# Kernel tuning notes

Hardware: AMD Instinct MI355X
Metric: run time of the kernel (lower is better)

The kernel has to match this reference:

```python
import jax, jax.numpy as jnp
import numpy as np

N = 16384          # nodes
E = 262144         # edges (before self-loops)
FIN_N, FIN_E = 768, 64
F, FE = 256, 128   # node/edge channels
H, C = 8, 32       # heads, per-head dim (H*C == F)
L = 2              # num GATv2 modules
NEG_SLOPE = 0.2


def layer_norm(x, g, b, eps=1e-5):
    mu = jnp.mean(x, axis=-1, keepdims=True)
    var = jnp.mean((x - mu) ** 2, axis=-1, keepdims=True)
    return (x - mu) * jax.lax.rsqrt(var + eps) * g + b


def segment_softmax(logits, seg, n):
    # logits: [Et, H], seg: [Et] destination node ids
    m = jax.ops.segment_max(logits, seg, num_segments=n)
    m = jnp.where(jnp.isfinite(m), m, 0.0)
    e = jnp.exp(logits - m[seg])
    s = jax.ops.segment_sum(e, seg, num_segments=n)
    return e / (s[seg] + 1e-16)


def setup_inputs() -> dict:
    key = jax.random.key(0)
    ks = jax.random.split(key, 20)
    inp = {
        "node_feats": jax.random.normal(ks[0], (N, FIN_N), jnp.float32),
        "edge_index": jax.random.randint(ks[1], (2, E), 0, N, dtype=jnp.int32),
        "edge_attr": jax.random.normal(ks[2], (E, FIN_E), jnp.float32),
        # input projections (bias=False)
        "init_node_w": jax.random.normal(ks[3], (F, FIN_N), jnp.float32) * 0.02,
        "init_edge_w": jax.random.normal(ks[4], (FE, FIN_E), jnp.float32) * 0.02,
        # per-layer GATv2 params, stacked on leading layer dim L
        "lin_l_w": jax.random.normal(ks[5], (L, H * C, F), jnp.float32) * 0.05,
        "lin_l_b": jnp.zeros((L, H * C), jnp.float32),
        "lin_r_w": jax.random.normal(ks[6], (L, H * C, F), jnp.float32) * 0.05,
        "lin_r_b": jnp.zeros((L, H * C), jnp.float32),
        "lin_edge_w": jax.random.normal(ks[7], (L, H * C, FE), jnp.float32) * 0.05,
        "att": jax.random.normal(ks[8], (L, H, C), jnp.float32) * 0.05,
        "gat_bias": jnp.zeros((L, H * C), jnp.float32),
        # block params
        "ln1_g": jnp.ones((L, F), jnp.float32), "ln1_b": jnp.zeros((L, F), jnp.float32),
        "mlp_w1": jax.random.normal(ks[9], (L, 2 * F, F), jnp.float32) * 0.05,
        "mlp_w2": jax.random.normal(ks[10], (L, F, 2 * F), jnp.float32) * 0.05,
        "ln2_g": jnp.ones((L, F), jnp.float32), "ln2_b": jnp.zeros((L, F), jnp.float32),
    }
    return inp


def _gatv2_module(x, src, dst, e_emb, p, l, n):
    # e_emb: [Et, H, C] already projected edge embeddings (incl. self-loops)
    x_l = (x @ p["lin_l_w"][l].T + p["lin_l_b"][l]).reshape(n, H, C)
    x_r = (x @ p["lin_r_w"][l].T + p["lin_r_b"][l]).reshape(n, H, C)
    m = x_l[src] + x_r[dst] + e_emb                    # [Et, H, C]
    g = jnp.where(m >= 0, m, NEG_SLOPE * m)            # leaky_relu(0.2)
    logits = jnp.einsum('ehc,hc->eh', g, p["att"][l])
    alpha = segment_softmax(logits, dst, n)            # [Et, H]
    out = jax.ops.segment_sum(alpha[:, :, None] * x_l[src], dst, num_segments=n)
    out = out.reshape(n, H * C) + p["gat_bias"][l]
    # residual -> LN -> MLP -> residual -> LN  (dropout=0, eval mode)
    h = layer_norm(x + out, p["ln1_g"][l], p["ln1_b"][l])
    y = jax.nn.gelu(h @ p["mlp_w1"][l].T, approximate=False) @ p["mlp_w2"][l].T
    return layer_norm(h + y, p["ln2_g"][l], p["ln2_b"][l])


def reference(node_feats, edge_index, edge_attr, init_node_w, init_edge_w,
              lin_l_w, lin_l_b, lin_r_w, lin_r_b, lin_edge_w, att, gat_bias,
              ln1_g, ln1_b, mlp_w1, mlp_w2, ln2_g, ln2_b):
    p = dict(lin_l_w=lin_l_w, lin_l_b=lin_l_b, lin_r_w=lin_r_w, lin_r_b=lin_r_b,
             lin_edge_w=lin_edge_w, att=att, gat_bias=gat_bias, ln1_g=ln1_g,
             ln1_b=ln1_b, mlp_w1=mlp_w1, mlp_w2=mlp_w2, ln2_g=ln2_g, ln2_b=ln2_b)
    x = node_feats @ init_node_w.T                     # [N, F]
    ea = edge_attr @ init_edge_w.T                     # [E, FE]
    src, dst = edge_index[0], edge_index[1]
    # add self loops with fill_value='mean' (mean of incoming edge_attr per node)
    cnt = jax.ops.segment_sum(jnp.ones((E,), ea.dtype), dst, num_segments=N)
    loop_attr = jax.ops.segment_sum(ea, dst, num_segments=N) / jnp.maximum(cnt, 1.0)[:, None]
    ea_all = jnp.concatenate([ea, loop_attr], axis=0)  # [E+N, FE]
    ar = jnp.arange(N, dtype=src.dtype)
    src_all = jnp.concatenate([src, ar])
    dst_all = jnp.concatenate([dst, ar])
    for l in range(L):
        e_emb = (ea_all @ lin_edge_w[l].T).reshape(-1, H, C)
        x = _gatv2_module(x, src_all, dst_all, e_emb, p, l, N)
    return x
```

## Files before the change

### kernel.cpp

```cpp
#include <hip/hip_runtime.h>

typedef unsigned short u16;
typedef __attribute__((ext_vector_type(8))) short s8v;
typedef __attribute__((ext_vector_type(4))) float f4v;

#define NN 16384
#define EE 262144
#define ET (EE + NN)
#define NTILES (ET / 64)

__device__ __forceinline__ float bfu(u16 h){ return __uint_as_float((unsigned)h << 16); }
__device__ __forceinline__ u16 f2bf(float f){
  unsigned u = __float_as_uint(f);
  unsigned r = u + 0x7FFFu + ((u >> 16) & 1u);
  return (u16)(r >> 16);
}
__device__ __forceinline__ float ldf(const void* p, size_t i, int isbf){
  return isbf ? bfu(((const u16*)p)[i]) : ((const float*)p)[i];
}
__device__ __forceinline__ float gelu_f(float x){ return 0.5f*x*(1.0f+erff(x*0.7071067811865475f)); }

__device__ __forceinline__ uint4 load8bf(const void* p, size_t eoff, int isbf){
  if (isbf) return *(const uint4*)((const u16*)p + eoff);
  const float* f = (const float*)p + eoff;
  uint4 r;
  r.x = (unsigned)f2bf(f[0]) | ((unsigned)f2bf(f[1])<<16);
  r.y = (unsigned)f2bf(f[2]) | ((unsigned)f2bf(f[3])<<16);
  r.z = (unsigned)f2bf(f[4]) | ((unsigned)f2bf(f[5])<<16);
  r.w = (unsigned)f2bf(f[6]) | ((unsigned)f2bf(f[7])<<16);
  return r;
}

__global__ void k_detect(const void* nf, int* flag)
{
  int t = threadIdx.x;
  const float* f = (const float*)nf;
  int cnt = 0;
  for (int i = t; i < 4096; i += 256) {
    float a = fabsf(f[i]);
    if (a > 1e-5f && a < 100.0f) cnt++;
  }
  __shared__ int s[256];
  s[t] = cnt; __syncthreads();
  for (int st = 128; st > 0; st >>= 1) { if (t < st) s[t] += s[t+st]; __syncthreads(); }
  if (t == 0) *flag = (s[0] < 2048) ? 1 : 0;
}

template<int ACT, int CFMT>
__global__ __launch_bounds__(256)
void mfma_gemm(const void* __restrict__ A, int a_fmt,
               const void* __restrict__ B1, size_t b1off,
               const void* __restrict__ B2, size_t b2off, int nsplit,
               const void* __restrict__ bias1, const void* __restrict__ bias2,
               size_t bioff, int has_bias,
               void* __restrict__ C, int M, int N, int K,
               const int* __restrict__ dflag)
{
  int isbf = *dflag;
  int af = (a_fmt == 2) ? isbf : a_fmt;
  __shared__ u16 As[128*40];
  __shared__ u16 Bs[128*40];
  int bm = blockIdx.y*128, bn = blockIdx.x*128;
  int t = threadIdx.x;
  int w = t>>6, lane = t&63, l4 = lane&15, quad = lane>>4;
  int wm = w>>1, wn = w&1;
  f4v zero = {0.f,0.f,0.f,0.f};
  f4v acc[4][4];
  #pragma unroll
  for (int i=0;i<4;i++)
    #pragma unroll
    for (int j=0;j<4;j++) acc[i][j] = zero;

  for (int k0 = 0; k0 < K; k0 += 32) {
    __syncthreads();
    #pragma unroll
    for (int it = 0; it < 2; ++it) {
      int sid = t + it*256;
      int row = sid >> 2, sk = sid & 3;
      *(uint4*)&As[row*40 + sk*8] = load8bf(A, (size_t)(bm+row)*K + k0 + sk*8, af);
      int col = bn + row;
      uint4 vb;
      if (col < nsplit) vb = load8bf(B1, b1off + (size_t)col*K + k0 + sk*8, isbf);
      else              vb = load8bf(B2, b2off + (size_t)(col-nsplit)*K + k0 + sk*8, isbf);
      *(uint4*)&Bs[row*40 + sk*8] = vb;
    }
    __syncthreads();
    s8v a[4], b[4];
    #pragma unroll
    for (int i=0;i<4;i++) a[i] = *(const s8v*)&As[(wm*64 + i*16 + l4)*40 + quad*8];
    #pragma unroll
    for (int j=0;j<4;j++) b[j] = *(const s8v*)&Bs[(wn*64 + j*16 + l4)*40 + quad*8];
    #pragma unroll
    for (int i=0;i<4;i++)
      #pragma unroll
      for (int j=0;j<4;j++)
        acc[i][j] = __builtin_amdgcn_mfma_f32_16x16x32_bf16(a[i], b[j], acc[i][j], 0,0,0);
  }
  #pragma unroll
  for (int i=0;i<4;i++)
    #pragma unroll
    for (int j=0;j<4;j++) {
      int col = bn + wn*64 + j*16 + l4;
      float bv = 0.f;
      if (has_bias) bv = (col < nsplit) ? ldf(bias1, bioff + col, isbf)
                                        : ldf(bias2, bioff + col - nsplit, isbf);
      #pragma unroll
      for (int r=0;r<4;r++) {
        int row = bm + wm*64 + i*16 + quad*4 + r;
        float v = acc[i][j][r] + bv;
        if (ACT==1) v = gelu_f(v);
        if (CFMT==1) ((u16*)C)[(size_t)row*N + col] = f2bf(v);
        else         ((float*)C)[(size_t)row*N + col] = v;
      }
    }
}

__global__ void k_count(const int* __restrict__ dst, int* __restrict__ deg)
{
  int e = blockIdx.x*256 + threadIdx.x;
  if (e >= ET) return;
  int d = (e < EE) ? dst[e] : (e - EE);
  atomicAdd(&deg[d], 1);
}

__global__ void k_scan(const int* __restrict__ deg, int* __restrict__ rowstart)
{
  __shared__ int csum[256];
  int t = threadIdx.x;
  int s = 0;
  for (int i=0;i<64;i++) s += deg[t*64+i];
  csum[t] = s;
  __syncthreads();
  if (t == 0) {
    int r = 0;
    for (int i=0;i<256;i++){ int v = csum[i]; csum[i] = r; r += v; }
    rowstart[NN] = r;
  }
  __syncthreads();
  int b = csum[t];
  for (int i=0;i<64;i++){ rowstart[t*64+i] = b; b += deg[t*64+i]; }
}

__global__ void k_scatter(const int* __restrict__ dst, const int* __restrict__ rowstart,
                          int* __restrict__ fill, int* __restrict__ csr)
{
  int e = blockIdx.x*256 + threadIdx.x;
  if (e >= ET) return;
  int d = (e < EE) ? dst[e] : (e - EE);
  int pos = rowstart[d] + atomicAdd(&fill[d], 1);
  csr[pos] = e;
}

__global__ void k_loopmean(const int* __restrict__ csr, const int* __restrict__ rowstart,
                           const void* __restrict__ edge_attr, u16* __restrict__ loopmean,
                           const int* __restrict__ dflag)
{
  int isbf = *dflag;
  int n = blockIdx.x, j = threadIdx.x;
  int s = rowstart[n], e1 = rowstart[n+1];
  float sum = 0.f; int cnt = 0;
  for (int p = s; p < e1; ++p) {
    int eid = csr[p];
    if (eid < EE) { sum += ldf(edge_attr, (size_t)eid*64 + j, isbf); cnt++; }
  }
  loopmean[(size_t)n*64 + j] = f2bf(sum / (float)max(cnt, 1));
}

__global__ void k_wc(const void* __restrict__ We, const void* __restrict__ iew,
                     u16* __restrict__ Wcb, const int* __restrict__ dflag)
{
  int isbf = *dflag;
  int idx = blockIdx.x*256 + threadIdx.x;
  int j = idx & 63, c = (idx >> 6) & 255, l = idx >> 14;
  float s = 0.f;
  for (int k=0;k<128;k++) s += ldf(We, ((size_t)l*256 + c)*128 + k, isbf) * ldf(iew, (size_t)k*64 + j, isbf);
  Wcb[idx] = f2bf(s);
}

__global__ __launch_bounds__(256)
void k_elogits(const int* __restrict__ src, const int* __restrict__ dst,
               const u16* __restrict__ Wcb, const u16* __restrict__ xlr,
               const void* __restrict__ edge_attr, const u16* __restrict__ loopmean,
               const void* __restrict__ att, size_t att_off,
               float* __restrict__ logits, const int* __restrict__ dflag)
{
  int isbf = *dflag;
  __shared__ u16 WcF[32*64*8];
  __shared__ u16 attr_s[64*72];
  __shared__ float satt[256];
  __shared__ int ssrc[64], sdst[64];

  int t = threadIdx.x;
  int w = t>>6, lane = t&63, l4 = lane&15, quad = lane>>4;

  satt[t] = ldf(att, att_off + t, isbf);
  #pragma unroll
  for (int f = 0; f < 8; ++f) {
    int fr = w + f*4;
    int i = fr >> 1, ks = fr & 1;
    *(uint4*)&WcF[(fr*64 + lane)*8] = *(const uint4*)&Wcb[(size_t)(16*i + l4)*64 + ks*32 + quad*8];
  }

  f4v zero = {0.f,0.f,0.f,0.f};
  for (int tile = blockIdx.x; tile < NTILES; tile += gridDim.x) {
    int e0 = tile*64;
    __syncthreads();
    if (t < 64) {
      int e = e0 + t;
      ssrc[t] = (e < EE) ? src[e] : (e - EE);
      sdst[t] = (e < EE) ? dst[e] : (e - EE);
    }
    {
      int er = t >> 2, part = t & 3;
      int e = e0 + er;
      uint4 v0, v1;
      if (e < EE) {
        v0 = load8bf(edge_attr, (size_t)e*64 + part*16,     isbf);
        v1 = load8bf(edge_attr, (size_t)e*64 + part*16 + 8, isbf);
      } else {
        v0 = *(const uint4*)&loopmean[(size_t)(e-EE)*64 + part*16];
        v1 = *(const uint4*)&loopmean[(size_t)(e-EE)*64 + part*16 + 8];
      }
      *(uint4*)&attr_s[er*72 + part*16]     = v0;
      *(uint4*)&attr_s[er*72 + part*16 + 8] = v1;
    }
    __syncthreads();

    s8v b0 = *(const s8v*)&attr_s[(w*16 + l4)*72 + quad*8];
    s8v b1 = *(const s8v*)&attr_s[(w*16 + l4)*72 + 32 + quad*8];
    f4v acc[16];
    #pragma unroll
    for (int i=0;i<16;++i){
      s8v a0 = *(const s8v*)&WcF[((2*i  )*64 + lane)*8];
      s8v a1 = *(const s8v*)&WcF[((2*i+1)*64 + lane)*8];
      acc[i] = __builtin_amdgcn_mfma_f32_16x16x32_bf16(a0, b0, zero, 0,0,0);
      acc[i] = __builtin_amdgcn_mfma_f32_16x16x32_bf16(a1, b1, acc[i], 0,0,0);
    }

    int me = w*16 + l4;
    int sn = ssrc[me], dn = sdst[me];
    float ph[8] = {0.f,0.f,0.f,0.f,0.f,0.f,0.f,0.f};
    #pragma unroll
    for (int i=0;i<16;++i){
      uint2 xlv = *(const uint2*)&xlr[(size_t)sn*512 +       i*16 + quad*4];
      uint2 xrv = *(const uint2*)&xlr[(size_t)dn*512 + 256 + i*16 + quad*4];
      float4 av = *(const float4*)&satt[i*16 + quad*4];
      float m0 = acc[i][0] + bfu((u16)(xlv.x & 0xffff)) + bfu((u16)(xrv.x & 0xffff));
      float m1 = acc[i][1] + bfu((u16)(xlv.x >> 16))    + bfu((u16)(xrv.x >> 16));
      float m2 = acc[i][2] + bfu((u16)(xlv.y & 0xffff)) + bfu((u16)(xrv.y & 0xffff));
      float m3 = acc[i][3] + bfu((u16)(xlv.y >> 16))    + bfu((u16)(xrv.y >> 16));
      float g0 = fmaxf(m0, 0.2f*m0), g1 = fmaxf(m1, 0.2f*m1);
      float g2 = fmaxf(m2, 0.2f*m2), g3 = fmaxf(m3, 0.2f*m3);
      ph[i>>1] += av.x*g0 + av.y*g1 + av.z*g2 + av.w*g3;
    }
    #pragma unroll
    for (int h=0;h<8;++h){
      ph[h] += __shfl_xor(ph[h], 16);
      ph[h] += __shfl_xor(ph[h], 32);
    }
    if (quad == 0){
      float4 lo = {ph[0], ph[1], ph[2], ph[3]};
      float4 hi = {ph[4], ph[5], ph[6], ph[7]};
      *(float4*)&logits[(size_t)(e0 + me)*8]     = lo;
      *(float4*)&logits[(size_t)(e0 + me)*8 + 4] = hi;
    }
  }
}

__global__ __launch_bounds__(256)
void k_aggln(const int* __restrict__ csr, const int* __restrict__ rowstart, const int* __restrict__ src,
             const float* __restrict__ logits, const u16* __restrict__ xlr, const float* __restrict__ xbuf,
             const void* __restrict__ gat_bias, const void* __restrict__ ln1g, const void* __restrict__ ln1b,
             size_t poff, float* __restrict__ hbuf, const int* __restrict__ dflag)
{
  int isbf = *dflag;
  int lane = threadIdx.x & 63, wid = threadIdx.x >> 6;
  int n = blockIdx.x*4 + wid;
  int s = rowstart[n], deg = rowstart[n+1] - s;
  int myh = lane >> 3;
  float mrun = -3.0e38f, lrun = 0.f;
  float a0=0.f, a1=0.f, a2=0.f, a3=0.f;

  for (int c0 = 0; c0 < deg; c0 += 64) {
    int idx = s + c0 + lane; if (idx >= ET) idx = ET-1;
    int ev = csr[idx];
    int sv = (ev < EE) ? src[ev] : (ev - EE);
    int lim = min(64, deg - c0);
    for (int j = 0; j < lim; ++j) {
      int eid = __shfl(ev, j);
      int sn  = __shfl(sv, j);
      float lg = logits[(size_t)eid*8 + myh];
      uint2 xv = *(const uint2*)&xlr[(size_t)sn*512 + 4*lane];
      float mn = fmaxf(mrun, lg);
      float sc = __expf(mrun - mn);
      float wv = __expf(lg - mn);
      mrun = mn;
      lrun = lrun*sc + wv;
      a0 = a0*sc + wv*bfu((u16)(xv.x & 0xffff));
      a1 = a1*sc + wv*bfu((u16)(xv.x >> 16));
      a2 = a2*sc + wv*bfu((u16)(xv.y & 0xffff));
      a3 = a3*sc + wv*bfu((u16)(xv.y >> 16));
    }
  }
  float inv = 1.f/(lrun + 1e-16f);
  int c = 4*lane;
  float4 res = *(const float4*)&xbuf[(size_t)n*256 + c];
  float o0 = a0*inv + ldf(gat_bias, poff+c+0, isbf) + res.x;
  float o1 = a1*inv + ldf(gat_bias, poff+c+1, isbf) + res.y;
  float o2 = a2*inv + ldf(gat_bias, poff+c+2, isbf) + res.z;
  float o3 = a3*inv + ldf(gat_bias, poff+c+3, isbf) + res.w;

  float v = o0+o1+o2+o3;
  #pragma unroll
  for (int off=1; off<64; off<<=1) v += __shfl_xor(v, off);
  float mu = v * (1.f/256.f);
  float d0=o0-mu, d1=o1-mu, d2=o2-mu, d3=o3-mu;
  float v2 = d0*d0+d1*d1+d2*d2+d3*d3;
  #pragma unroll
  for (int off=1; off<64; off<<=1) v2 += __shfl_xor(v2, off);
  float wn = rsqrtf(v2*(1.f/256.f) + 1e-5f);
  float4 outv;
  outv.x = d0*wn*ldf(ln1g, poff+c+0, isbf) + ldf(ln1b, poff+c+0, isbf);
  outv.y = d1*wn*ldf(ln1g, poff+c+1, isbf) + ldf(ln1b, poff+c+1, isbf);
  outv.z = d2*wn*ldf(ln1g, poff+c+2, isbf) + ldf(ln1b, poff+c+2, isbf);
  outv.w = d3*wn*ldf(ln1g, poff+c+3, isbf) + ldf(ln1b, poff+c+3, isbf);
  *(float4*)&hbuf[(size_t)n*256 + c] = outv;
}

__global__ __launch_bounds__(256)
void k_ln_add(const float* __restrict__ a, const u16* __restrict__ b2,
              const void* __restrict__ gg, const void* __restrict__ bb, size_t poff,
              float* __restrict__ out, const int* __restrict__ dflag)
{
  int isbf = *dflag;
  int n = blockIdx.x, t = threadIdx.x;
  __shared__ float r[256];
  float x = a[(size_t)n*256 + t] + bfu(b2[(size_t)n*256 + t]);
  r[t] = x; __syncthreads();
  for (int st = 128; st > 0; st >>= 1) { if (t < st) r[t] += r[t+st]; __syncthreads(); }
  float mu = r[0] * (1.f/256.f);
  __syncthreads();
  float d = x - mu;
  r[t] = d*d; __syncthreads();
  for (int st = 128; st > 0; st >>= 1) { if (t < st) r[t] += r[t+st]; __syncthreads(); }
  float var = r[0] * (1.f/256.f);
  out[(size_t)n*256 + t] = d * rsqrtf(var + 1e-5f) * ldf(gg, poff + t, isbf) + ldf(bb, poff + t, isbf);
}

__global__ void k_out(const float* __restrict__ x, void* __restrict__ out, const int* __restrict__ dflag)
{
  int isbf = *dflag;
  int i = blockIdx.x*256 + threadIdx.x;
  if (isbf) ((u16*)out)[i] = f2bf(x[i]);
  else      ((float*)out)[i] = x[i];
}

extern "C" void kernel_launch(void* const* d_in, const int* in_sizes, int n_in,
                              void* d_out, int out_size, void* d_ws, size_t ws_size,
                              hipStream_t stream)
{
  const void* node_feats = d_in[0];
  const int*  edge_index = (const int*)d_in[1];
  const void* edge_attr  = d_in[2];
  const void* init_node_w= d_in[3];
  const void* init_edge_w= d_in[4];
  const void* lin_l_w    = d_in[5];
  const void* lin_l_b    = d_in[6];
  const void* lin_r_w    = d_in[7];
  const void* lin_r_b    = d_in[8];
  const void* lin_edge_w = d_in[9];
  const void* att        = d_in[10];
  const void* gat_bias   = d_in[11];
  const void* ln1_g      = d_in[12];
  const void* ln1_b      = d_in[13];
  const void* mlp_w1     = d_in[14];
  const void* mlp_w2     = d_in[15];
  const void* ln2_g      = d_in[16];
  const void* ln2_b      = d_in[17];

  const int* srcp = edge_index;
  const int* dstp = edge_index + EE;

  char* p = (char*)d_ws;
  auto alloc = [&](size_t bytes) { void* r = (void*)p; p += (bytes + 255) & ~(size_t)255; return r; };
  int*   dflag   = (int*)alloc(256);
  int*   deg     = (int*)alloc((size_t)NN*4);
  int*   rowstart= (int*)alloc((size_t)(NN+1)*4);
  int*   fill    = (int*)alloc((size_t)NN*4);
  int*   csr     = (int*)alloc((size_t)ET*4);
  u16*   Wcb     = (u16*)alloc((size_t)2*256*64*2);
  u16*   loopmean= (u16*)alloc((size_t)NN*64*2);
  float* logits  = (float*)alloc((size_t)ET*8*4);
  float* xbuf    = (float*)alloc((size_t)NN*256*4);
  float* hbuf    = (float*)alloc((size_t)NN*256*4);
  u16*   xlr     = (u16*)alloc((size_t)NN*512*2);
  u16*   ymid    = xlr;
  u16*   y2      = (u16*)d_out;

  hipMemsetAsync(deg,  0, (size_t)NN*4, stream);
  hipMemsetAsync(fill, 0, (size_t)NN*4, stream);

  k_detect <<<1, 256, 0, stream>>>(node_feats, dflag);

  k_count  <<<(ET+255)/256, 256, 0, stream>>>(dstp, deg);
  k_scan   <<<1, 256, 0, stream>>>(deg, rowstart);
  k_scatter<<<(ET+255)/256, 256, 0, stream>>>(dstp, rowstart, fill, csr);
  k_loopmean<<<NN, 64, 0, stream>>>(csr, rowstart, edge_attr, loopmean, dflag);
  k_wc     <<<128, 256, 0, stream>>>(lin_edge_w, init_edge_w, Wcb, dflag);

  mfma_gemm<0,0><<<dim3(2,128), 256, 0, stream>>>(node_feats, 2, init_node_w, 0, init_node_w, 0, 1<<29,
                                                  nullptr, nullptr, 0, 0, xbuf, NN, 256, 768, dflag);

  for (int l = 0; l < 2; ++l) {
    size_t wo = (size_t)l*256*256;
    size_t bo = (size_t)l*256;
    mfma_gemm<0,1><<<dim3(4,128), 256, 0, stream>>>(xbuf, 0, lin_l_w, wo, lin_r_w, wo, 256,
                                                    lin_l_b, lin_r_b, bo, 1, xlr, NN, 512, 256, dflag);
    k_elogits<<<768, 256, 0, stream>>>(srcp, dstp, Wcb + (size_t)l*256*64, xlr,
                                       edge_attr, loopmean, att, (size_t)l*256, logits, dflag);
    k_aggln<<<NN/4, 256, 0, stream>>>(csr, rowstart, srcp, logits, xlr, xbuf,
                                      gat_bias, ln1_g, ln1_b, bo, hbuf, dflag);
    mfma_gemm<1,1><<<dim3(4,128), 256, 0, stream>>>(hbuf, 0, mlp_w1, (size_t)l*512*256, mlp_w1, 0, 1<<29,
                                                    nullptr, nullptr, 0, 0, ymid, NN, 512, 256, dflag);
    mfma_gemm<0,1><<<dim3(2,128), 256, 0, stream>>>(ymid, 1, mlp_w2, (size_t)l*256*512, mlp_w2, 0, 1<<29,
                                                    nullptr, nullptr, 0, 0, y2, NN, 256, 512, dflag);
    k_ln_add<<<NN, 256, 0, stream>>>(hbuf, y2, ln2_g, ln2_b, bo, xbuf, dflag);
  }

  k_out<<<(NN*256)/256, 256, 0, stream>>>(xbuf, d_out, dflag);
}
```

Baseline: 778.7 us.

## Compute edge logits in CSR order and use two-pass softmax in aggregation

The scatter step now also records the source and destination node of each CSR slot. Edge logits are computed and stored in destination-sorted order, so the edge kernel drops its shared-memory staging and barriers, and the aggregation kernel reads logits contiguously. Aggregation replaces the online rescaling softmax with a separate max pass followed by plain exp-weighted accumulation, which saves one exp and several multiplies per edge. The costs are gathered edge_attr reads in the logits kernel, extra srcof/dstof buffers, and a second pass over each node's logits. The logits grid size also changes.

```diff
diff --git a/kernel.cpp b/kernel.cpp
--- a/kernel.cpp
+++ b/kernel.cpp
@@ -141,14 +141,17 @@
   for (int i=0;i<64;i++){ rowstart[t*64+i] = b; b += deg[t*64+i]; }
 }
 
-__global__ void k_scatter(const int* __restrict__ dst, const int* __restrict__ rowstart,
-                          int* __restrict__ fill, int* __restrict__ csr)
+__global__ void k_scatter(const int* __restrict__ dst, const int* __restrict__ src,
+                          const int* __restrict__ rowstart, int* __restrict__ fill,
+                          int* __restrict__ csr, int* __restrict__ srcof, int* __restrict__ dstof)
 {
   int e = blockIdx.x*256 + threadIdx.x;
   if (e >= ET) return;
   int d = (e < EE) ? dst[e] : (e - EE);
   int pos = rowstart[d] + atomicAdd(&fill[d], 1);
   csr[pos] = e;
+  srcof[pos] = (e < EE) ? src[e] : (e - EE);
+  dstof[pos] = d;
 }
 
 __global__ void k_loopmean(const int* __restrict__ csr, const int* __restrict__ rowstart,
@@ -178,7 +181,7 @@
 }
 
 __global__ __launch_bounds__(256)
-void k_elogits(const int* __restrict__ src, const int* __restrict__ dst,
+void k_elogits(const int* __restrict__ csr, const int* __restrict__ srcof, const int* __restrict__ dstof,
                const u16* __restrict__ Wcb, const u16* __restrict__ xlr,
                const void* __restrict__ edge_attr, const u16* __restrict__ loopmean,
                const void* __restrict__ att, size_t att_off,
@@ -186,9 +189,7 @@
 {
   int isbf = *dflag;
   __shared__ u16 WcF[32*64*8];
-  __shared__ u16 attr_s[64*72];
   __shared__ float satt[256];
-  __shared__ int ssrc[64], sdst[64];
 
   int t = threadIdx.x;
   int w = t>>6, lane = t&63, l4 = lane&15, quad = lane>>4;
@@ -200,34 +201,25 @@
     int i = fr >> 1, ks = fr & 1;
     *(uint4*)&WcF[(fr*64 + lane)*8] = *(const uint4*)&Wcb[(size_t)(16*i + l4)*64 + ks*32 + quad*8];
   }
+  __syncthreads();
 
   f4v zero = {0.f,0.f,0.f,0.f};
   for (int tile = blockIdx.x; tile < NTILES; tile += gridDim.x) {
-    int e0 = tile*64;
-    __syncthreads();
-    if (t < 64) {
-      int e = e0 + t;
-      ssrc[t] = (e < EE) ? src[e] : (e - EE);
-      sdst[t] = (e < EE) ? dst[e] : (e - EE);
-    }
-    {
-      int er = t >> 2, part = t & 3;
-      int e = e0 + er;
-      uint4 v0, v1;
-      if (e < EE) {
-        v0 = load8bf(edge_attr, (size_t)e*64 + part*16,     isbf);
-        v1 = load8bf(edge_attr, (size_t)e*64 + part*16 + 8, isbf);
-      } else {
-        v0 = *(const uint4*)&loopmean[(size_t)(e-EE)*64 + part*16];
-        v1 = *(const uint4*)&loopmean[(size_t)(e-EE)*64 + part*16 + 8];
-      }
-      *(uint4*)&attr_s[er*72 + part*16]     = v0;
-      *(uint4*)&attr_s[er*72 + part*16 + 8] = v1;
-    }
-    __syncthreads();
-
-    s8v b0 = *(const s8v*)&attr_s[(w*16 + l4)*72 + quad*8];
-    s8v b1 = *(const s8v*)&attr_s[(w*16 + l4)*72 + 32 + quad*8];
+    int p  = tile*64 + w*16 + l4;
+    int eid = csr[p];
+    int sn = srcof[p], dn = dstof[p];
+
+    uint4 b0u, b1u;
+    if (eid < EE) {
+      b0u = load8bf(edge_attr, (size_t)eid*64 + quad*8,      isbf);
+      b1u = load8bf(edge_attr, (size_t)eid*64 + 32 + quad*8, isbf);
+    } else {
+      b0u = *(const uint4*)&loopmean[(size_t)(eid-EE)*64 + quad*8];
+      b1u = *(const uint4*)&loopmean[(size_t)(eid-EE)*64 + 32 + quad*8];
+    }
+    s8v b0 = *(const s8v*)&b0u;
+    s8v b1 = *(const s8v*)&b1u;
+
     f4v acc[16];
     #pragma unroll
     for (int i=0;i<16;++i){
@@ -237,8 +229,6 @@
       acc[i] = __builtin_amdgcn_mfma_f32_16x16x32_bf16(a1, b1, acc[i], 0,0,0);
     }
 
-    int me = w*16 + l4;
-    int sn = ssrc[me], dn = sdst[me];
     float ph[8] = {0.f,0.f,0.f,0.f,0.f,0.f,0.f,0.f};
     #pragma unroll
     for (int i=0;i<16;++i){
@@ -261,14 +251,14 @@
     if (quad == 0){
       float4 lo = {ph[0], ph[1], ph[2], ph[3]};
       float4 hi = {ph[4], ph[5], ph[6], ph[7]};
-      *(float4*)&logits[(size_t)(e0 + me)*8]     = lo;
-      *(float4*)&logits[(size_t)(e0 + me)*8 + 4] = hi;
+      *(float4*)&logits[(size_t)p*8]     = lo;
+      *(float4*)&logits[(size_t)p*8 + 4] = hi;
     }
   }
 }
 
 __global__ __launch_bounds__(256)
-void k_aggln(const int* __restrict__ csr, const int* __restrict__ rowstart, const int* __restrict__ src,
+void k_aggln(const int* __restrict__ rowstart, const int* __restrict__ srcof,
              const float* __restrict__ logits, const u16* __restrict__ xlr, const float* __restrict__ xbuf,
              const void* __restrict__ gat_bias, const void* __restrict__ ln1g, const void* __restrict__ ln1b,
              size_t poff, float* __restrict__ hbuf, const int* __restrict__ dflag)
@@ -278,28 +268,40 @@
   int n = blockIdx.x*4 + wid;
   int s = rowstart[n], deg = rowstart[n+1] - s;
   int myh = lane >> 3;
-  float mrun = -3.0e38f, lrun = 0.f;
-  float a0=0.f, a1=0.f, a2=0.f, a3=0.f;
-
+
+  float m0=-3e38f,m1=-3e38f,m2=-3e38f,m3=-3e38f,m4=-3e38f,m5=-3e38f,m6=-3e38f,m7=-3e38f;
+  for (int j = lane; j < deg; j += 64) {
+    const float4* lp = (const float4*)&logits[(size_t)(s+j)*8];
+    float4 a = lp[0], b = lp[1];
+    m0=fmaxf(m0,a.x); m1=fmaxf(m1,a.y); m2=fmaxf(m2,a.z); m3=fmaxf(m3,a.w);
+    m4=fmaxf(m4,b.x); m5=fmaxf(m5,b.y); m6=fmaxf(m6,b.z); m7=fmaxf(m7,b.w);
+  }
+  #pragma unroll
+  for (int off=1; off<64; off<<=1) {
+    m0=fmaxf(m0,__shfl_xor(m0,off)); m1=fmaxf(m1,__shfl_xor(m1,off));
+    m2=fmaxf(m2,__shfl_xor(m2,off)); m3=fmaxf(m3,__shfl_xor(m3,off));
+    m4=fmaxf(m4,__shfl_xor(m4,off)); m5=fmaxf(m5,__shfl_xor(m5,off));
+    m6=fmaxf(m6,__shfl_xor(m6,off)); m7=fmaxf(m7,__shfl_xor(m7,off));
+  }
+  float mh = m0;
+  if (myh==1) mh=m1; if (myh==2) mh=m2; if (myh==3) mh=m3;
+  if (myh==4) mh=m4; if (myh==5) mh=m5; if (myh==6) mh=m6; if (myh==7) mh=m7;
+
+  float lrun = 0.f, a0=0.f, a1=0.f, a2=0.f, a3=0.f;
   for (int c0 = 0; c0 < deg; c0 += 64) {
     int idx = s + c0 + lane; if (idx >= ET) idx = ET-1;
-    int ev = csr[idx];
-    int sv = (ev < EE) ? src[ev] : (ev - EE);
+    int sv = srcof[idx];
     int lim = min(64, deg - c0);
     for (int j = 0; j < lim; ++j) {
-      int eid = __shfl(ev, j);
-      int sn  = __shfl(sv, j);
-      float lg = logits[(size_t)eid*8 + myh];
+      int sn = __shfl(sv, j);
+      float lg = logits[(size_t)(s + c0 + j)*8 + myh];
+      float wv = __expf(lg - mh);
       uint2 xv = *(const uint2*)&xlr[(size_t)sn*512 + 4*lane];
-      float mn = fmaxf(mrun, lg);
-      float sc = __expf(mrun - mn);
-      float wv = __expf(lg - mn);
-      mrun = mn;
-      lrun = lrun*sc + wv;
-      a0 = a0*sc + wv*bfu((u16)(xv.x & 0xffff));
-      a1 = a1*sc + wv*bfu((u16)(xv.x >> 16));
-      a2 = a2*sc + wv*bfu((u16)(xv.y & 0xffff));
-      a3 = a3*sc + wv*bfu((u16)(xv.y >> 16));
+      lrun += wv;
+      a0 += wv*bfu((u16)(xv.x & 0xffff));
+      a1 += wv*bfu((u16)(xv.x >> 16));
+      a2 += wv*bfu((u16)(xv.y & 0xffff));
+      a3 += wv*bfu((u16)(xv.y >> 16));
     }
   }
   float inv = 1.f/(lrun + 1e-16f);
@@ -388,6 +390,8 @@
   int*   rowstart= (int*)alloc((size_t)(NN+1)*4);
   int*   fill    = (int*)alloc((size_t)NN*4);
   int*   csr     = (int*)alloc((size_t)ET*4);
+  int*   srcof   = (int*)alloc((size_t)ET*4);
+  int*   dstof   = (int*)alloc((size_t)ET*4);
   u16*   Wcb     = (u16*)alloc((size_t)2*256*64*2);
   u16*   loopmean= (u16*)alloc((size_t)NN*64*2);
   float* logits  = (float*)alloc((size_t)ET*8*4);
@@ -404,7 +408,7 @@
 
   k_count  <<<(ET+255)/256, 256, 0, stream>>>(dstp, deg);
   k_scan   <<<1, 256, 0, stream>>>(deg, rowstart);
-  k_scatter<<<(ET+255)/256, 256, 0, stream>>>(dstp, rowstart, fill, csr);
+  k_scatter<<<(ET+255)/256, 256, 0, stream>>>(dstp, srcp, rowstart, fill, csr, srcof, dstof);
   k_loopmean<<<NN, 64, 0, stream>>>(csr, rowstart, edge_attr, loopmean, dflag);
   k_wc     <<<128, 256, 0, stream>>>(lin_edge_w, init_edge_w, Wcb, dflag);
 
@@ -416,9 +420,9 @@
     size_t bo = (size_t)l*256;
     mfma_gemm<0,1><<<dim3(4,128), 256, 0, stream>>>(xbuf, 0, lin_l_w, wo, lin_r_w, wo, 256,
                                                     lin_l_b, lin_r_b, bo, 1, xlr, NN, 512, 256, dflag);
-    k_elogits<<<768, 256, 0, stream>>>(srcp, dstp, Wcb + (size_t)l*256*64, xlr,
-                                       edge_attr, loopmean, att, (size_t)l*256, logits, dflag);
-    k_aggln<<<NN/4, 256, 0, stream>>>(csr, rowstart, srcp, logits, xlr, xbuf,
+    k_elogits<<<1088, 256, 0, stream>>>(csr, srcof, dstof, Wcb + (size_t)l*256*64, xlr,
+                                        edge_attr, loopmean, att, (size_t)l*256, logits, dflag);
+    k_aggln<<<NN/4, 256, 0, stream>>>(rowstart, srcof, logits, xlr, xbuf,
                                       gat_bias, ln1_g, ln1_b, bo, hbuf, dflag);
     mfma_gemm<1,1><<<dim3(4,128), 256, 0, stream>>>(hbuf, 0, mlp_w1, (size_t)l*512*256, mlp_w1, 0, 1<<29,
                                                     nullptr, nullptr, 0, 0, ymid, NN, 512, 256, dflag);
```

Result: slower. 876.9 us (+12.6%).
